# Kernel optimization log

Hardware: AMD Instinct MI355X
Metric: run time of the kernel (lower is better)

The kernel has to match this reference:

```python
import jax, jax.numpy as jnp
import numpy as np

N = 100000   # nodes
E = 1600000  # edges (avg degree 16)
F = 128      # input features
H = 64       # hidden_dim
C = 10       # num_classes
G = 128      # graphs in batch
EPS = 1e-5   # BatchNorm eps


def setup_inputs() -> dict:
    key = jax.random.key(0)
    ks = jax.random.split(key, 24)
    d = {}
    d['x'] = jax.random.normal(ks[0], (N, F), jnp.float32)
    d['edge_index'] = jax.random.randint(ks[1], (2, E), 0, N)
    d['batch'] = jnp.sort(jax.random.randint(ks[2], (N,), 0, G))
    # SAGEConv1: lin_l (aggregated, with bias) + lin_r (root, no bias)
    d['W1l'] = jax.random.normal(ks[3], (F, H), jnp.float32) * 0.05
    d['W1r'] = jax.random.normal(ks[4], (F, H), jnp.float32) * 0.05
    d['b1'] = jnp.zeros((H,), jnp.float32)
    # SAGEConv2
    d['W2l'] = jax.random.normal(ks[5], (H, H), jnp.float32) * 0.1
    d['W2r'] = jax.random.normal(ks[6], (H, H), jnp.float32) * 0.1
    d['b2'] = jnp.zeros((H,), jnp.float32)
    # BatchNorm (eval mode: running stats)
    for i, (kg, kb, km, kv) in enumerate([(7, 8, 9, 10), (11, 12, 13, 14), (15, 16, 17, 18)], 1):
        d[f'bn{i}_g'] = jax.random.uniform(ks[kg], (H,), jnp.float32, 0.5, 1.5)
        d[f'bn{i}_b'] = jax.random.normal(ks[kb], (H,), jnp.float32) * 0.1
        d[f'bn{i}_m'] = jax.random.normal(ks[km], (H,), jnp.float32) * 0.1
        d[f'bn{i}_v'] = jax.random.uniform(ks[kv], (H,), jnp.float32, 0.5, 1.5)
    # classifier head
    d['Wc1'] = jax.random.normal(ks[19], (H, H), jnp.float32) * 0.1
    d['bc1'] = jnp.zeros((H,), jnp.float32)
    d['Wc2'] = jax.random.normal(ks[20], (H, C), jnp.float32) * 0.1
    d['bc2'] = jnp.zeros((C,), jnp.float32)
    return d


def _bn(x, g, b, m, v):
    return (x - m) * jax.lax.rsqrt(v + EPS) * g + b


def _sage(x, src, dst, Wl, Wr, b):
    # mean aggregation of source-node features at destination nodes
    msum = jax.ops.segment_sum(x[src], dst, num_segments=N)          # [N, d]
    cnt = jax.ops.segment_sum(jnp.ones((E,), x.dtype), dst, num_segments=N)
    mean = msum / jnp.maximum(cnt, 1.0)[:, None]
    return mean @ Wl + b + x @ Wr


def reference(x, edge_index, batch,
              W1l, W1r, b1, W2l, W2r, b2,
              bn1_g, bn1_b, bn1_m, bn1_v,
              bn2_g, bn2_b, bn2_m, bn2_v,
              Wc1, bc1, bn3_g, bn3_b, bn3_m, bn3_v,
              Wc2, bc2):
    src, dst = edge_index[0], edge_index[1]
    h = _sage(x, src, dst, W1l, W1r, b1)
    h = jax.nn.relu(_bn(h, bn1_g, bn1_b, bn1_m, bn1_v))
    h = _sage(h, src, dst, W2l, W2r, b2)
    h = jax.nn.relu(_bn(h, bn2_g, bn2_b, bn2_m, bn2_v))
    # global mean pool over graphs
    gsum = jax.ops.segment_sum(h, batch, num_segments=G)             # [G, H]
    gcnt = jax.ops.segment_sum(jnp.ones((N,), h.dtype), batch, num_segments=G)
    g = gsum / jnp.maximum(gcnt, 1.0)[:, None]
    # classifier head (eval: dropout is identity)
    g = jax.nn.relu(_bn(g @ Wc1 + bc1, bn3_g, bn3_b, bn3_m, bn3_v))
    logits = g @ Wc2 + bc2
    return jax.nn.log_softmax(logits, axis=1)
```

## Files before the change

### kernel.cpp

```cpp
#include <hip/hip_runtime.h>
#include <hip/hip_bf16.h>
#include <math.h>

#define NN 100000
#define NE 1600000
#define FF 128
#define HH 64
#define CC 10
#define GG 128
#define BN_EPS 1e-5f

#define BNODES 64
#define NB 1563
#define PBLK 128
#define ECHUNK 12500
#define MHIST (NB * PBLK)
#define NSCAN 782
#define SCOL_CAP 2048

#define PNODES 16
#define POOL_BLOCKS 1563

typedef short v8bf __attribute__((ext_vector_type(8)));
typedef float v4f  __attribute__((ext_vector_type(4)));

__device__ inline ushort f2b(float x) {
    __hip_bfloat16 h = __float2bfloat16(x);
    return *reinterpret_cast<ushort*>(&h);
}
__device__ inline float b2f(ushort u) {
    return __uint_as_float(((unsigned)u) << 16);
}
__device__ inline float blo(unsigned u) { return __uint_as_float(u << 16); }
__device__ inline float bhi(unsigned u) { return __uint_as_float(u & 0xffff0000u); }

__device__ inline void sw_one(const float* __restrict__ W, ushort* __restrict__ o,
                              int t, int K) {
    const int lane = t & 63, nt = (t >> 6) & 3, ks = t >> 8;
    const int m = lane & 15, quad = lane >> 4;
#pragma unroll
    for (int j = 0; j < 8; ++j) {
        const int kk = ks * 32 + quad * 8 + j;
        const int cc = nt * 16 + m;
        o[t * 8 + j] = f2b(W[kk * 64 + cc]);
    }
}

__global__ __launch_bounds__(256) void prep_kernel(const float* __restrict__ W1l,
                                                   const float* __restrict__ W1r,
                                                   const float* __restrict__ W2l,
                                                   const float* __restrict__ W2r,
                                                   ushort* __restrict__ w1ls,
                                                   ushort* __restrict__ w1rs,
                                                   ushort* __restrict__ w2ls,
                                                   ushort* __restrict__ w2rs,
                                                   float* __restrict__ gz) {
    const int t = blockIdx.x * 256 + threadIdx.x;
    if (t < 1024) {
        sw_one(W1l, w1ls, t, FF);
        sw_one(W1r, w1rs, t, FF);
    } else if (t < 1536) {
        sw_one(W2l, w2ls, t - 1024, HH);
        sw_one(W2r, w2rs, t - 1024, HH);
    } else {
        for (int i = t - 1536; i < GG * 64 + GG; i += 512) gz[i] = 0.f;
    }
}

template<int K, int TPB, bool AF32>
__global__ __launch_bounds__(256) void gemm_mfma(const void* __restrict__ Xv,
                                                 const ushort* __restrict__ Bl,
                                                 const ushort* __restrict__ Br,
                                                 ushort* __restrict__ Yl,
                                                 ushort* __restrict__ Yr) {
    constexpr int KS = K / 32;
    const int lane  = threadIdx.x & 63;
    const int wave  = threadIdx.x >> 6;
    const int nhalf = wave & 1;
    const int rsub  = wave >> 1;
    const int m = lane & 15, quad = lane >> 4;

    v8bf bl[KS][2], br[KS][2];
#pragma unroll
    for (int ks = 0; ks < KS; ++ks)
#pragma unroll
        for (int nt = 0; nt < 2; ++nt) {
            const int nti = nhalf * 2 + nt;
            bl[ks][nt] = *(const v8bf*)(Bl + ((size_t)(ks * 4 + nti) * 64 + lane) * 8);
            br[ks][nt] = *(const v8bf*)(Br + ((size_t)(ks * 4 + nti) * 64 + lane) * 8);
        }

    for (int it = 0; it < TPB; ++it) {
        const int bt = blockIdx.x * TPB + it;
        const int row0 = bt * 32 + rsub * 16;
        if (row0 >= NN) return;
        const v4f z = {0.f, 0.f, 0.f, 0.f};
        v4f accl[2] = {z, z}, accr[2] = {z, z};
#pragma unroll
        for (int ks = 0; ks < KS; ++ks) {
            v8bf a;
            if (AF32) {
                const float* xrow = (const float*)Xv + (size_t)(row0 + m) * K + quad * 8 + ks * 32;
                const float4 a0 = *(const float4*)(xrow);
                const float4 a1 = *(const float4*)(xrow + 4);
                a[0] = (short)f2b(a0.x); a[1] = (short)f2b(a0.y);
                a[2] = (short)f2b(a0.z); a[3] = (short)f2b(a0.w);
                a[4] = (short)f2b(a1.x); a[5] = (short)f2b(a1.y);
                a[6] = (short)f2b(a1.z); a[7] = (short)f2b(a1.w);
            } else {
                const ushort* xrow = (const ushort*)Xv + (size_t)(row0 + m) * K + quad * 8 + ks * 32;
                a = *(const v8bf*)xrow;
            }
#pragma unroll
            for (int nt = 0; nt < 2; ++nt) {
                accl[nt] = __builtin_amdgcn_mfma_f32_16x16x32_bf16(a, bl[ks][nt], accl[nt], 0, 0, 0);
                accr[nt] = __builtin_amdgcn_mfma_f32_16x16x32_bf16(a, br[ks][nt], accr[nt], 0, 0, 0);
            }
        }
#pragma unroll
        for (int nt = 0; nt < 2; ++nt) {
            const int cc = nhalf * 32 + nt * 16 + m;
#pragma unroll
            for (int r = 0; r < 4; ++r) {
                const size_t off = (size_t)(row0 + quad * 4 + r) * 64 + cc;
                Yl[off] = f2b(accl[nt][r]);
                Yr[off] = f2b(accr[nt][r]);
            }
        }
    }
}

__global__ __launch_bounds__(1024) void edge_hist(const int* __restrict__ dst,
                                                  int* __restrict__ hist) {
    __shared__ int h[NB];
    for (int i = threadIdx.x; i < NB; i += 1024) h[i] = 0;
    __syncthreads();
    const int e0 = blockIdx.x * ECHUNK;
    for (int e = e0 + threadIdx.x; e < e0 + ECHUNK; e += 1024)
        atomicAdd(&h[dst[e] >> 6], 1);
    __syncthreads();
    for (int i = threadIdx.x; i < NB; i += 1024)
        hist[i * PBLK + blockIdx.x] = h[i];
}

__global__ __launch_bounds__(256) void scan_block(const int* __restrict__ cnt,
                                                  int* __restrict__ rp,
                                                  int* __restrict__ bsum) {
    __shared__ int s[256];
    const int tid = threadIdx.x;
    const int i = blockIdx.x * 256 + tid;
    const int v = (i < MHIST) ? cnt[i] : 0;
    s[tid] = v;
    __syncthreads();
    for (int off = 1; off < 256; off <<= 1) {
        int t = (tid >= off) ? s[tid - off] : 0;
        __syncthreads();
        s[tid] += t;
        __syncthreads();
    }
    if (i < MHIST) rp[i] = s[tid] - v;
    if (tid == 255) bsum[blockIdx.x] = s[255];
}

__global__ __launch_bounds__(256) void scan_bsums(const int* __restrict__ bsum,
                                                  int* __restrict__ boff) {
    __shared__ int s[256];
    const int tid = threadIdx.x;
    int v[4];
    int tot = 0;
#pragma unroll
    for (int j = 0; j < 4; ++j) {
        const int idx = tid * 4 + j;
        v[j] = (idx < NSCAN) ? bsum[idx] : 0;
        tot += v[j];
    }
    s[tid] = tot;
    __syncthreads();
    for (int off = 1; off < 256; off <<= 1) {
        int t = (tid >= off) ? s[tid - off] : 0;
        __syncthreads();
        s[tid] += t;
        __syncthreads();
    }
    int run = s[tid] - tot;
#pragma unroll
    for (int j = 0; j < 4; ++j) {
        const int idx = tid * 4 + j;
        if (idx < NSCAN) boff[idx] = run;
        run += v[j];
    }
}

__global__ __launch_bounds__(1024) void edge_scatter(const int* __restrict__ src,
                                                     const int* __restrict__ dst,
                                                     const int* __restrict__ goffs,
                                                     const int* __restrict__ boff,
                                                     int* __restrict__ pairs) {
    __shared__ int cur[NB];
    for (int i = threadIdx.x; i < NB; i += 1024) {
        const int idx = i * PBLK + blockIdx.x;
        cur[i] = goffs[idx] + boff[idx >> 8];
    }
    __syncthreads();
    const int e0 = blockIdx.x * ECHUNK;
    for (int e = e0 + threadIdx.x; e < e0 + ECHUNK; e += 1024) {
        const int s = src[e];
        const int d = dst[e];
        const int pos = atomicAdd(&cur[d >> 6], 1);
        pairs[pos] = (s << 6) | (d & (BNODES - 1));
    }
}

__global__ __launch_bounds__(256) void spmm_sorted(const int* __restrict__ goffs,
                                                   const int* __restrict__ boff,
                                                   const int* __restrict__ pairs,
                                                   const ushort* __restrict__ Yl,
                                                   const ushort* __restrict__ Yr,
                                                   const float* __restrict__ bias,
                                                   const float* __restrict__ bng,
                                                   const float* __restrict__ bnb,
                                                   const float* __restrict__ bnm,
                                                   const float* __restrict__ bnv,
                                                   ushort* __restrict__ outp) {
    __shared__ int scol[SCOL_CAP];
    __shared__ int deg[BNODES];
    __shared__ int loffs[BNODES];
    __shared__ int fill[BNODES];
    const int tid = threadIdx.x;
    const int b = blockIdx.x;

    if (tid < BNODES) { deg[tid] = 0; fill[tid] = 0; }
    __syncthreads();

    const int beg = goffs[b * PBLK] + boff[b >> 1];
    int end = (b == NB - 1) ? NE : goffs[(b + 1) * PBLK] + boff[(b + 1) >> 1];
    if (end - beg > SCOL_CAP) end = beg + SCOL_CAP;

    int pv[8];
    int npv = 0;
    for (int i = beg + tid; i < end; i += 256) {
        const int v = pairs[i];
        pv[npv++] = v;
        atomicAdd(&deg[v & (BNODES - 1)], 1);
    }
    __syncthreads();

    if (tid < BNODES) loffs[tid] = deg[tid];
    __syncthreads();
    for (int s = 1; s < BNODES; s <<= 1) {
        int v = 0;
        if (tid < BNODES && tid >= s) v = loffs[tid - s];
        __syncthreads();
        if (tid < BNODES) loffs[tid] += v;
        __syncthreads();
    }

    for (int j = 0; j < npv; ++j) {
        const int v = pv[j];
        const int dl = v & (BNODES - 1);
        const int pos = (loffs[dl] - deg[dl]) + atomicAdd(&fill[dl], 1);
        scol[pos] = v >> 6;
    }
    __syncthreads();

    const int wv = tid >> 6, lane = tid & 63;
    const int grp = lane >> 3, subl = lane & 7;

    float biasj[8], scj[8], mj[8], bbj[8];
#pragma unroll
    for (int j = 0; j < 8; ++j) {
        const int ch = subl * 8 + j;
        biasj[j] = bias[ch];
        scj[j] = bng[ch] * rsqrtf(bnv[ch] + BN_EPS);
        mj[j] = bnm[ch];
        bbj[j] = bnb[ch];
    }

    for (int i = 0; i < 2; ++i) {
        const int nl = wv * 16 + i * 8 + grp;
        const int node = b * BNODES + nl;
        if (node >= NN) continue;
        const int dg = deg[nl];
        const int nbeg = loffs[nl] - dg;
        const int nend = nbeg + dg;
        float a[8] = {0.f, 0.f, 0.f, 0.f, 0.f, 0.f, 0.f, 0.f};
        float c[8] = {0.f, 0.f, 0.f, 0.f, 0.f, 0.f, 0.f, 0.f};
        int e = nbeg;
        for (; e + 1 < nend; e += 2) {
            const int s0 = scol[e];
            const int s1 = scol[e + 1];
            const uint4 r0 = *(const uint4*)(Yl + (size_t)s0 * 64 + subl * 8);
            const uint4 r1 = *(const uint4*)(Yl + (size_t)s1 * 64 + subl * 8);
            a[0] += blo(r0.x); a[1] += bhi(r0.x); a[2] += blo(r0.y); a[3] += bhi(r0.y);
            a[4] += blo(r0.z); a[5] += bhi(r0.z); a[6] += blo(r0.w); a[7] += bhi(r0.w);
            c[0] += blo(r1.x); c[1] += bhi(r1.x); c[2] += blo(r1.y); c[3] += bhi(r1.y);
            c[4] += blo(r1.z); c[5] += bhi(r1.z); c[6] += blo(r1.w); c[7] += bhi(r1.w);
        }
        if (e < nend) {
            const int s0 = scol[e];
            const uint4 r0 = *(const uint4*)(Yl + (size_t)s0 * 64 + subl * 8);
            a[0] += blo(r0.x); a[1] += bhi(r0.x); a[2] += blo(r0.y); a[3] += bhi(r0.y);
            a[4] += blo(r0.z); a[5] += bhi(r0.z); a[6] += blo(r0.w); a[7] += bhi(r0.w);
        }
        const float inv = 1.0f / fmaxf((float)dg, 1.0f);
        const uint4 yr = *(const uint4*)(Yr + (size_t)node * 64 + subl * 8);
        float hj[8];
        hj[0] = (a[0] + c[0]) * inv + biasj[0] + blo(yr.x);
        hj[1] = (a[1] + c[1]) * inv + biasj[1] + bhi(yr.x);
        hj[2] = (a[2] + c[2]) * inv + biasj[2] + blo(yr.y);
        hj[3] = (a[3] + c[3]) * inv + biasj[3] + bhi(yr.y);
        hj[4] = (a[4] + c[4]) * inv + biasj[4] + blo(yr.z);
        hj[5] = (a[5] + c[5]) * inv + biasj[5] + bhi(yr.z);
        hj[6] = (a[6] + c[6]) * inv + biasj[6] + blo(yr.w);
        hj[7] = (a[7] + c[7]) * inv + biasj[7] + bhi(yr.w);
        unsigned ow[4];
#pragma unroll
        for (int j = 0; j < 4; ++j) {
            const float o0 = fmaxf((hj[2 * j] - mj[2 * j]) * scj[2 * j] + bbj[2 * j], 0.0f);
            const float o1 = fmaxf((hj[2 * j + 1] - mj[2 * j + 1]) * scj[2 * j + 1] + bbj[2 * j + 1], 0.0f);
            ow[j] = (unsigned)f2b(o0) | ((unsigned)f2b(o1) << 16);
        }
        uint4 o;
        o.x = ow[0]; o.y = ow[1]; o.z = ow[2]; o.w = ow[3];
        *(uint4*)(outp + (size_t)node * 64 + subl * 8) = o;
    }
}

__global__ __launch_bounds__(256) void pool_seg(const ushort* __restrict__ h,
                                                const int* __restrict__ batch,
                                                float* __restrict__ gsum,
                                                float* __restrict__ gcnt) {
    const int wave = blockIdx.x * 4 + (threadIdx.x >> 6);
    const int lane = threadIdx.x & 63;
    const int n0 = wave * PNODES;
    if (n0 >= NN) return;
    const int n1 = (n0 + PNODES < NN) ? n0 + PNODES : NN;
    int g = batch[n0];
    float acc = 0.f, c = 0.f;
#pragma unroll 4
    for (int n = n0; n < n1; ++n) {
        const int b = batch[n];
        if (b != g) {
            atomicAdd(&gsum[g * 64 + lane], acc);
            if (lane == 0) atomicAdd(&gcnt[g], c);
            acc = 0.f; c = 0.f; g = b;
        }
        acc += b2f(h[(size_t)n * 64 + lane]);
        c += 1.0f;
    }
    atomicAdd(&gsum[g * 64 + lane], acc);
    if (lane == 0) atomicAdd(&gcnt[g], c);
}

__global__ __launch_bounds__(64) void head_kernel(const float* __restrict__ gsum,
                                                  const float* __restrict__ gcnt,
                                                  const float* __restrict__ Wc1,
                                                  const float* __restrict__ bc1,
                                                  const float* __restrict__ g3,
                                                  const float* __restrict__ b3,
                                                  const float* __restrict__ m3,
                                                  const float* __restrict__ v3,
                                                  const float* __restrict__ Wc2,
                                                  const float* __restrict__ bc2,
                                                  float* __restrict__ out) {
    __shared__ float sg[64];
    __shared__ float st[64];
    __shared__ float sl[10];
    __shared__ float sls;
    const int b = blockIdx.x;
    const int c = threadIdx.x;
    sg[c] = gsum[b * 64 + c] / fmaxf(gcnt[b], 1.0f);
    __syncthreads();
    float acc = bc1[c];
#pragma unroll
    for (int k = 0; k < 64; ++k) acc += sg[k] * Wc1[k * 64 + c];
    const float sc = g3[c] * rsqrtf(v3[c] + BN_EPS);
    st[c] = fmaxf((acc - m3[c]) * sc + b3[c], 0.0f);
    __syncthreads();
    if (c < CC) {
        float lg = bc2[c];
#pragma unroll
        for (int k = 0; k < 64; ++k) lg += st[k] * Wc2[k * CC + c];
        sl[c] = lg;
    }
    __syncthreads();
    if (c == 0) {
        float mx = sl[0];
        for (int i = 1; i < CC; ++i) mx = fmaxf(mx, sl[i]);
        float s = 0.f;
        for (int i = 0; i < CC; ++i) s += expf(sl[i] - mx);
        sls = mx + logf(s);
    }
    __syncthreads();
    if (c < CC) out[b * CC + c] = sl[c] - sls;
}

extern "C" void kernel_launch(void* const* d_in, const int* in_sizes, int n_in,
                              void* d_out, int out_size, void* d_ws, size_t ws_size,
                              hipStream_t stream) {
    const float* x    = (const float*)d_in[0];
    const int*   ei   = (const int*)d_in[1];
    const int*   batch= (const int*)d_in[2];
    const float* W1l  = (const float*)d_in[3];
    const float* W1r  = (const float*)d_in[4];
    const float* b1   = (const float*)d_in[5];
    const float* W2l  = (const float*)d_in[6];
    const float* W2r  = (const float*)d_in[7];
    const float* b2   = (const float*)d_in[8];
    const float* bn1g = (const float*)d_in[9];
    const float* bn1b = (const float*)d_in[10];
    const float* bn1m = (const float*)d_in[11];
    const float* bn1v = (const float*)d_in[12];
    const float* bn2g = (const float*)d_in[13];
    const float* bn2b = (const float*)d_in[14];
    const float* bn2m = (const float*)d_in[15];
    const float* bn2v = (const float*)d_in[16];
    const float* bn3g = (const float*)d_in[17];
    const float* bn3b = (const float*)d_in[18];
    const float* bn3m = (const float*)d_in[19];
    const float* bn3v = (const float*)d_in[20];
    const float* Wc1  = (const float*)d_in[21];
    const float* bc1  = (const float*)d_in[22];
    const float* Wc2  = (const float*)d_in[23];
    const float* bc2  = (const float*)d_in[24];
    float* out = (float*)d_out;

    const int* src = ei;
    const int* dst = ei + NE;

    char* p = (char*)d_ws;
    ushort* yl   = (ushort*)p;                 p += (size_t)NN * 64 * 2;
    ushort* yr   = (ushort*)p;                 p += (size_t)NN * 64 * 2;
    ushort* hbuf = (ushort*)p;                 p += (size_t)NN * 64 * 2;
    int*    pairs= (int*)p;                    p += (size_t)NE * 4;
    int*    hist = (int*)p;                    p += (size_t)MHIST * 4;
    int*    goffs= (int*)p;                    p += (size_t)MHIST * 4;
    int*    bsum = (int*)p;                    p += 1024 * 4;
    int*    boff = (int*)p;                    p += 1024 * 4;
    ushort* w1ls = (ushort*)p;                 p += (size_t)FF * 64 * 2;
    ushort* w1rs = (ushort*)p;                 p += (size_t)FF * 64 * 2;
    ushort* w2ls = (ushort*)p;                 p += (size_t)HH * 64 * 2;
    ushort* w2rs = (ushort*)p;                 p += (size_t)HH * 64 * 2;
    float* gsum  = (float*)p;                  p += (size_t)GG * 64 * 4;
    float* gcnt  = gsum + GG * 64;             p += (size_t)GG * 4;

    edge_hist<<<PBLK, 1024, 0, stream>>>(dst, hist);
    scan_block<<<NSCAN, 256, 0, stream>>>(hist, goffs, bsum);
    scan_bsums<<<1, 256, 0, stream>>>(bsum, boff);
    edge_scatter<<<PBLK, 1024, 0, stream>>>(src, dst, goffs, boff, pairs);

    prep_kernel<<<8, 256, 0, stream>>>(W1l, W1r, W2l, W2r, w1ls, w1rs, w2ls, w2rs, gsum);

    gemm_mfma<FF, 2, true><<<1563, 256, 0, stream>>>((const void*)x, w1ls, w1rs, yl, yr);
    spmm_sorted<<<NB, 256, 0, stream>>>(goffs, boff, pairs, yl, yr, b1,
                                        bn1g, bn1b, bn1m, bn1v, hbuf);

    gemm_mfma<HH, 2, false><<<1563, 256, 0, stream>>>((const void*)hbuf, w2ls, w2rs, yl, yr);
    spmm_sorted<<<NB, 256, 0, stream>>>(goffs, boff, pairs, yl, yr, b2,
                                        bn2g, bn2b, bn2m, bn2v, hbuf);

    pool_seg<<<POOL_BLOCKS, 256, 0, stream>>>(hbuf, batch, gsum, gcnt);
    head_kernel<<<GG, 64, 0, stream>>>(gsum, gcnt, Wc1, bc1,
                                       bn3g, bn3b, bn3m, bn3v, Wc2, bc2, out);
}
```

Measured before the change: 289.4 us.

## Replace global histogram/scan/scatter with per-chunk local edge sort

```diff
diff --git a/kernel.cpp b/kernel.cpp
--- a/kernel.cpp
+++ b/kernel.cpp
@@ -12,10 +12,8 @@
 
 #define BNODES 64
 #define NB 1563
-#define PBLK 128
-#define ECHUNK 12500
-#define MHIST (NB * PBLK)
-#define NSCAN 782
+#define PBLK 256
+#define ECHUNK 6250
 #define SCOL_CAP 2048
 
 #define PNODES 16
@@ -130,89 +128,52 @@
     }
 }
 
-__global__ __launch_bounds__(1024) void edge_hist(const int* __restrict__ dst,
-                                                  int* __restrict__ hist) {
-    __shared__ int h[NB];
-    for (int i = threadIdx.x; i < NB; i += 1024) h[i] = 0;
-    __syncthreads();
-    const int e0 = blockIdx.x * ECHUNK;
-    for (int e = e0 + threadIdx.x; e < e0 + ECHUNK; e += 1024)
-        atomicAdd(&h[dst[e] >> 6], 1);
-    __syncthreads();
-    for (int i = threadIdx.x; i < NB; i += 1024)
-        hist[i * PBLK + blockIdx.x] = h[i];
-}
-
-__global__ __launch_bounds__(256) void scan_block(const int* __restrict__ cnt,
-                                                  int* __restrict__ rp,
-                                                  int* __restrict__ bsum) {
-    __shared__ int s[256];
+__global__ __launch_bounds__(1024) void edge_sort(const int* __restrict__ src,
+                                                  const int* __restrict__ dst,
+                                                  int* __restrict__ lofs,
+                                                  int* __restrict__ pairs) {
+    __shared__ int lcnt[NB];
+    __shared__ int lpos[NB];
+    __shared__ int psum[1024];
     const int tid = threadIdx.x;
-    const int i = blockIdx.x * 256 + tid;
-    const int v = (i < MHIST) ? cnt[i] : 0;
-    s[tid] = v;
-    __syncthreads();
-    for (int off = 1; off < 256; off <<= 1) {
-        int t = (tid >= off) ? s[tid - off] : 0;
-        __syncthreads();
-        s[tid] += t;
-        __syncthreads();
-    }
-    if (i < MHIST) rp[i] = s[tid] - v;
-    if (tid == 255) bsum[blockIdx.x] = s[255];
-}
-
-__global__ __launch_bounds__(256) void scan_bsums(const int* __restrict__ bsum,
-                                                  int* __restrict__ boff) {
-    __shared__ int s[256];
-    const int tid = threadIdx.x;
-    int v[4];
-    int tot = 0;
-#pragma unroll
-    for (int j = 0; j < 4; ++j) {
-        const int idx = tid * 4 + j;
-        v[j] = (idx < NSCAN) ? bsum[idx] : 0;
-        tot += v[j];
-    }
-    s[tid] = tot;
-    __syncthreads();
-    for (int off = 1; off < 256; off <<= 1) {
-        int t = (tid >= off) ? s[tid - off] : 0;
-        __syncthreads();
-        s[tid] += t;
-        __syncthreads();
-    }
-    int run = s[tid] - tot;
-#pragma unroll
-    for (int j = 0; j < 4; ++j) {
-        const int idx = tid * 4 + j;
-        if (idx < NSCAN) boff[idx] = run;
-        run += v[j];
-    }
-}
-
-__global__ __launch_bounds__(1024) void edge_scatter(const int* __restrict__ src,
-                                                     const int* __restrict__ dst,
-                                                     const int* __restrict__ goffs,
-                                                     const int* __restrict__ boff,
-                                                     int* __restrict__ pairs) {
-    __shared__ int cur[NB];
-    for (int i = threadIdx.x; i < NB; i += 1024) {
-        const int idx = i * PBLK + blockIdx.x;
-        cur[i] = goffs[idx] + boff[idx >> 8];
-    }
-    __syncthreads();
-    const int e0 = blockIdx.x * ECHUNK;
-    for (int e = e0 + threadIdx.x; e < e0 + ECHUNK; e += 1024) {
+    const int b = blockIdx.x;
+    const int e0 = b * ECHUNK;
+
+    for (int i = tid; i < NB; i += 1024) lcnt[i] = 0;
+    __syncthreads();
+    for (int e = e0 + tid; e < e0 + ECHUNK; e += 1024)
+        atomicAdd(&lcnt[dst[e] >> 6], 1);
+    __syncthreads();
+
+    const int i0 = 2 * tid, i1 = 2 * tid + 1;
+    const int v0 = (i0 < NB) ? lcnt[i0] : 0;
+    const int v1 = (i1 < NB) ? lcnt[i1] : 0;
+    psum[tid] = v0 + v1;
+    __syncthreads();
+    for (int off = 1; off < 1024; off <<= 1) {
+        int t = (tid >= off) ? psum[tid - off] : 0;
+        __syncthreads();
+        psum[tid] += t;
+        __syncthreads();
+    }
+    const int base = psum[tid] - v0 - v1;
+    if (i0 < NB) lpos[i0] = base;
+    if (i1 < NB) lpos[i1] = base + v0;
+    __syncthreads();
+
+    for (int i = tid; i < NB; i += 1024) lofs[(size_t)b * NB + i] = lpos[i];
+    for (int i = tid; i < NB; i += 1024) lcnt[i] = lpos[i];
+    __syncthreads();
+
+    for (int e = e0 + tid; e < e0 + ECHUNK; e += 1024) {
         const int s = src[e];
         const int d = dst[e];
-        const int pos = atomicAdd(&cur[d >> 6], 1);
-        pairs[pos] = (s << 6) | (d & (BNODES - 1));
-    }
-}
-
-__global__ __launch_bounds__(256) void spmm_sorted(const int* __restrict__ goffs,
-                                                   const int* __restrict__ boff,
+        const int pos = atomicAdd(&lcnt[d >> 6], 1);
+        pairs[e0 + pos] = (s << 6) | (d & (BNODES - 1));
+    }
+}
+
+__global__ __launch_bounds__(256) void spmm_sorted(const int* __restrict__ lofs,
                                                    const int* __restrict__ pairs,
                                                    const ushort* __restrict__ Yl,
                                                    const ushort* __restrict__ Yr,
@@ -222,28 +183,42 @@
                                                    const float* __restrict__ bnm,
                                                    const float* __restrict__ bnv,
                                                    ushort* __restrict__ outp) {
+    __shared__ int scol2[SCOL_CAP];
     __shared__ int scol[SCOL_CAP];
     __shared__ int deg[BNODES];
     __shared__ int loffs[BNODES];
     __shared__ int fill[BNODES];
+    __shared__ int rbs[256];
+    __shared__ int total_s;
     const int tid = threadIdx.x;
     const int b = blockIdx.x;
 
     if (tid < BNODES) { deg[tid] = 0; fill[tid] = 0; }
-    __syncthreads();
-
-    const int beg = goffs[b * PBLK] + boff[b >> 1];
-    int end = (b == NB - 1) ? NE : goffs[(b + 1) * PBLK] + boff[(b + 1) >> 1];
-    if (end - beg > SCOL_CAP) end = beg + SCOL_CAP;
-
-    int pv[8];
-    int npv = 0;
-    for (int i = beg + tid; i < end; i += 256) {
-        const int v = pairs[i];
-        pv[npv++] = v;
+
+    const int lo = lofs[(size_t)tid * NB + b];
+    const int hi = (b == NB - 1) ? ECHUNK : lofs[(size_t)tid * NB + b + 1];
+    int len = hi - lo;
+    rbs[tid] = len;
+    __syncthreads();
+    for (int off = 1; off < 256; off <<= 1) {
+        int t = (tid >= off) ? rbs[tid - off] : 0;
+        __syncthreads();
+        rbs[tid] += t;
+        __syncthreads();
+    }
+    int rbase = rbs[tid] - len;
+    if (tid == 255) total_s = (rbs[255] > SCOL_CAP) ? SCOL_CAP : rbs[255];
+    if (rbase >= SCOL_CAP) len = 0;
+    else if (rbase + len > SCOL_CAP) len = SCOL_CAP - rbase;
+
+    const int gbase = tid * ECHUNK + lo;
+    for (int j = 0; j < len; ++j) {
+        const int v = pairs[gbase + j];
+        scol2[rbase + j] = v;
         atomicAdd(&deg[v & (BNODES - 1)], 1);
     }
     __syncthreads();
+    const int total = total_s;
 
     if (tid < BNODES) loffs[tid] = deg[tid];
     __syncthreads();
@@ -255,8 +230,8 @@
         __syncthreads();
     }
 
-    for (int j = 0; j < npv; ++j) {
-        const int v = pv[j];
+    for (int j = tid; j < total; j += 256) {
+        const int v = scol2[j];
         const int dl = v & (BNODES - 1);
         const int pos = (loffs[dl] - deg[dl]) + atomicAdd(&fill[dl], 1);
         scol[pos] = v >> 6;
@@ -433,10 +408,7 @@
     ushort* yr   = (ushort*)p;                 p += (size_t)NN * 64 * 2;
     ushort* hbuf = (ushort*)p;                 p += (size_t)NN * 64 * 2;
     int*    pairs= (int*)p;                    p += (size_t)NE * 4;
-    int*    hist = (int*)p;                    p += (size_t)MHIST * 4;
-    int*    goffs= (int*)p;                    p += (size_t)MHIST * 4;
-    int*    bsum = (int*)p;                    p += 1024 * 4;
-    int*    boff = (int*)p;                    p += 1024 * 4;
+    int*    lofs = (int*)p;                    p += (size_t)PBLK * NB * 4;
     ushort* w1ls = (ushort*)p;                 p += (size_t)FF * 64 * 2;
     ushort* w1rs = (ushort*)p;                 p += (size_t)FF * 64 * 2;
     ushort* w2ls = (ushort*)p;                 p += (size_t)HH * 64 * 2;
@@ -444,19 +416,16 @@
     float* gsum  = (float*)p;                  p += (size_t)GG * 64 * 4;
     float* gcnt  = gsum + GG * 64;             p += (size_t)GG * 4;
 
-    edge_hist<<<PBLK, 1024, 0, stream>>>(dst, hist);
-    scan_block<<<NSCAN, 256, 0, stream>>>(hist, goffs, bsum);
-    scan_bsums<<<1, 256, 0, stream>>>(bsum, boff);
-    edge_scatter<<<PBLK, 1024, 0, stream>>>(src, dst, goffs, boff, pairs);
+    edge_sort<<<PBLK, 1024, 0, stream>>>(src, dst, lofs, pairs);
 
     prep_kernel<<<8, 256, 0, stream>>>(W1l, W1r, W2l, W2r, w1ls, w1rs, w2ls, w2rs, gsum);
 
     gemm_mfma<FF, 2, true><<<1563, 256, 0, stream>>>((const void*)x, w1ls, w1rs, yl, yr);
-    spmm_sorted<<<NB, 256, 0, stream>>>(goffs, boff, pairs, yl, yr, b1,
+    spmm_sorted<<<NB, 256, 0, stream>>>(lofs, pairs, yl, yr, b1,
                                         bn1g, bn1b, bn1m, bn1v, hbuf);
 
     gemm_mfma<HH, 2, false><<<1563, 256, 0, stream>>>((const void*)hbuf, w2ls, w2rs, yl, yr);
-    spmm_sorted<<<NB, 256, 0, stream>>>(goffs, boff, pairs, yl, yr, b2,
+    spmm_sorted<<<NB, 256, 0, stream>>>(lofs, pairs, yl, yr, b2,
                                         bn2g, bn2b, bn2m, bn2v, hbuf);
 
     pool_seg<<<POOL_BLOCKS, 256, 0, stream>>>(hbuf, batch, gsum, gcnt);
```

New measurement: 317.8 us. 9.8% more time.
